# Performance work log

Hardware: AMD Instinct MI355X
Metric: run time of the kernel (lower is better)

The kernel has to match this reference:

```python
import jax, jax.numpy as jnp
import numpy as np

N_NODES = 20000
N_EDGES = 640000
D = 128


def setup_inputs() -> dict:
    key = jax.random.key(0)
    ks = jax.random.split(key, 8)
    scale = 1.0 / np.sqrt(D)
    x = jax.random.normal(ks[0], (N_NODES, D), dtype=jnp.float32)
    edge_index = jax.random.randint(ks[1], (2, N_EDGES), 0, N_NODES, dtype=jnp.int64)
    W1_rel = jax.random.normal(ks[2], (D, D), dtype=jnp.float32) * scale
    b1_rel = jnp.zeros((D,), dtype=jnp.float32)
    W1_root = jax.random.normal(ks[3], (D, D), dtype=jnp.float32) * scale
    W2_rel = jax.random.normal(ks[4], (D, D), dtype=jnp.float32) * scale
    b2_rel = jnp.zeros((D,), dtype=jnp.float32)
    W2_root = jax.random.normal(ks[5], (D, D), dtype=jnp.float32) * scale
    return {"x": x, "edge_index": edge_index,
            "W1_rel": W1_rel, "b1_rel": b1_rel, "W1_root": W1_root,
            "W2_rel": W2_rel, "b2_rel": b2_rel, "W2_root": W2_root}


def _graph_conv(x, src, dst, W_rel, b_rel, W_root):
    # sum-aggregate neighbor features: gather from src, scatter-add to dst
    agg = jax.ops.segment_sum(x[src], dst, num_segments=N_NODES)  # [N, D]
    # PyG GraphConv: lin_rel(agg) (with bias) + lin_root(x) (no bias)
    return agg @ W_rel + b_rel + x @ W_root


def reference(x, edge_index, W1_rel, b1_rel, W1_root, W2_rel, b2_rel, W2_root):
    src, dst = edge_index[0], edge_index[1]  # messages flow src (j) -> dst (i)
    h = jax.nn.relu(_graph_conv(x, src, dst, W1_rel, b1_rel, W1_root))
    out = _graph_conv(h, src, dst, W2_rel, b2_rel, W2_root)  # final ReLU stripped
    return out
```

## Files before the change

### kernel.cpp

```cpp
#include <hip/hip_runtime.h>

#define N_NODES 20000
#define N_EDGES 640000
#define D 128
#define CAP 128

typedef __attribute__((ext_vector_type(8))) short bf16x8;
typedef __attribute__((ext_vector_type(4))) float f32x4;

__device__ __forceinline__ short f2bf(float f) {
    union { float f; unsigned u; } un; un.f = f;
    unsigned r = un.u + 0x7fff + ((un.u >> 16) & 1);
    return (short)(r >> 16);
}
__device__ __forceinline__ float bflo(unsigned u) { return __uint_as_float(u << 16); }
__device__ __forceinline__ float bfhi(unsigned u) { return __uint_as_float(u & 0xffff0000u); }

__global__ __launch_bounds__(256) void prep_kernel(
    const float* __restrict__ x,
    const int* __restrict__ src, const int* __restrict__ dst,
    const float* __restrict__ W1_rel, const float* __restrict__ W1_root,
    const float* __restrict__ W2_rel, const float* __restrict__ W2_root,
    int* __restrict__ cnt, unsigned short* __restrict__ buckets,
    short* __restrict__ xb, short* __restrict__ wpk1, short* __restrict__ wpk2)
{
    const int b = blockIdx.x;
    const int tid = threadIdx.x;
    if (b < 625) {
        int e4 = b * 256 + tid;
        int4 s4 = ((const int4*)src)[e4];
        int4 d4 = ((const int4*)dst)[e4];
#pragma unroll
        for (int q = 0; q < 4; q++) {
            int d = (&d4.x)[q];
            int s = (&s4.x)[q];
            int p = atomicAdd(&cnt[d], 1);
            if (p < CAP) buckets[(d << 7) + p] = (unsigned short)s;
        }
    } else if (b < 3125) {
        int i = (b - 625) * 256 + tid;
        float4 v = ((const float4*)x)[i];
        ushort4 o;
        o.x = (unsigned short)f2bf(v.x);
        o.y = (unsigned short)f2bf(v.y);
        o.z = (unsigned short)f2bf(v.z);
        o.w = (unsigned short)f2bf(v.w);
        ((ushort4*)xb)[i] = o;
    } else {
        int pb  = b - 3125;
        int job = pb >> 4;
        int idx = (pb & 15) * 256 + tid;
        const float* Wrel  = job ? W2_rel  : W1_rel;
        const float* Wroot = job ? W2_root : W1_root;
        short* Wpk = job ? wpk2 : wpk1;
        int lane = idx & 63;
        int ct   = (idx >> 6) & 7;
        int t    = idx >> 9;
        const float* W = (t < 4) ? Wrel : Wroot;
        int k0  = (t & 3) * 32 + (lane >> 4) * 8;
        int col = ct * 16 + (lane & 15);
        bf16x8 pk;
#pragma unroll
        for (int j = 0; j < 8; j++)
            pk[j] = f2bf(W[(size_t)(k0 + j) * D + col]);
        ((bf16x8*)Wpk)[idx] = pk;
    }
}

__global__ __launch_bounds__(256) void aggregate_kernel(
    const short* __restrict__ xb,
    const int* __restrict__ cnt,
    const unsigned short* __restrict__ buckets,
    short* __restrict__ aggb)
{
    int node = blockIdx.x * 8 + (threadIdx.x >> 5);
    int lane = threadIdx.x & 31;
    int n = cnt[node];
    n = (n > CAP) ? CAP : n;
    uint2 idxpk = *(const uint2*)(buckets + (node << 7) + lane * 4);

    float4 acc = make_float4(0.f, 0.f, 0.f, 0.f);
    int i = 0;
    for (; i + 8 <= n; i += 8) {
        int baseLane = i >> 2;
        uint2 u[8];
#pragma unroll
        for (int q = 0; q < 8; q++) {
            unsigned word = __shfl((q & 2) ? idxpk.y : idxpk.x,
                                   baseLane + (q >> 2), 32);
            unsigned sidx = (q & 1) ? (word >> 16) : (word & 0xffffu);
            u[q] = *(const uint2*)(xb + (size_t)sidx * D + lane * 4);
        }
#pragma unroll
        for (int q = 0; q < 8; q++) {
            acc.x += bflo(u[q].x); acc.y += bfhi(u[q].x);
            acc.z += bflo(u[q].y); acc.w += bfhi(u[q].y);
        }
    }
    for (; i < n; i++) {
        unsigned word = __shfl((i & 2) ? idxpk.y : idxpk.x, i >> 2, 32);
        unsigned sidx = (i & 1) ? (word >> 16) : (word & 0xffffu);
        uint2 u0 = *(const uint2*)(xb + (size_t)sidx * D + lane * 4);
        acc.x += bflo(u0.x); acc.y += bfhi(u0.x);
        acc.z += bflo(u0.y); acc.w += bfhi(u0.y);
    }
    ushort4 o;
    o.x = (unsigned short)f2bf(acc.x);
    o.y = (unsigned short)f2bf(acc.y);
    o.z = (unsigned short)f2bf(acc.z);
    o.w = (unsigned short)f2bf(acc.w);
    *(ushort4*)(aggb + (size_t)node * D + lane * 4) = o;
}

template <bool RELU, bool OUT_BF16>
__global__ __launch_bounds__(128) void gemm_kernel(
    const short* __restrict__ aggb,
    const short* __restrict__ xb,
    const short* __restrict__ Wpk,
    const float* __restrict__ brel,
    void* __restrict__ outp)
{
    const int tid  = threadIdx.x;
    const int wave = tid >> 6;
    const int lane = tid & 63;
    const int quad = lane >> 4;
    const int l16  = lane & 15;
    const int row0 = blockIdx.x * 32 + wave * 16;

    f32x4 acc[8];
#pragma unroll
    for (int ct = 0; ct < 8; ct++) acc[ct] = (f32x4){0.f, 0.f, 0.f, 0.f};

    const short* arow_agg = aggb + (size_t)(row0 + l16) * D + quad * 8;
    const short* arow_x   = xb   + (size_t)(row0 + l16) * D + quad * 8;
    const bf16x8* wb = (const bf16x8*)Wpk + lane;

#pragma unroll
    for (int t = 0; t < 8; t++) {
        const short* arow = (t < 4) ? arow_agg : arow_x;
        bf16x8 a = *(const bf16x8*)(arow + (t & 3) * 32);
        const bf16x8* wt = wb + (size_t)t * 8 * 64;
#pragma unroll
        for (int ct = 0; ct < 8; ct++) {
            bf16x8 bfr = wt[ct * 64];
            acc[ct] = __builtin_amdgcn_mfma_f32_16x16x32_bf16(a, bfr, acc[ct], 0, 0, 0);
        }
    }

    const int orow = row0 + quad * 4;
#pragma unroll
    for (int ct = 0; ct < 8; ct++) {
        const int col = ct * 16 + l16;
        const float bias = brel[col];
#pragma unroll
        for (int r = 0; r < 4; r++) {
            float v = acc[ct][r] + bias;
            if (RELU) v = fmaxf(v, 0.f);
            if (OUT_BF16)
                ((short*)outp)[(size_t)(orow + r) * D + col] = f2bf(v);
            else
                ((float*)outp)[(size_t)(orow + r) * D + col] = v;
        }
    }
}

extern "C" void kernel_launch(void* const* d_in, const int* in_sizes, int n_in,
                              void* d_out, int out_size, void* d_ws, size_t ws_size,
                              hipStream_t stream) {
    const float* x       = (const float*)d_in[0];
    const int*   ei      = (const int*)  d_in[1];
    const float* W1_rel  = (const float*)d_in[2];
    const float* b1_rel  = (const float*)d_in[3];
    const float* W1_root = (const float*)d_in[4];
    const float* W2_rel  = (const float*)d_in[5];
    const float* b2_rel  = (const float*)d_in[6];
    const float* W2_root = (const float*)d_in[7];
    float* out = (float*)d_out;

    char* p = (char*)d_ws;
    short* xb   = (short*)p;  p += (size_t)N_NODES * D * 2;
    short* hb   = (short*)p;  p += (size_t)N_NODES * D * 2;
    short* aggb = (short*)p;  p += (size_t)N_NODES * D * 2;
    short* wpk1 = (short*)p;  p += 65536;
    short* wpk2 = (short*)p;  p += 65536;
    int*   cnt  = (int*)p;    p += (size_t)N_NODES * 4;
    unsigned short* buckets = (unsigned short*)p;

    const int* src = ei;
    const int* dst = ei + N_EDGES;

    const int aggblocks  = N_NODES / 8;
    const int gemmblocks = N_NODES / 32;

    hipMemsetAsync(cnt, 0, (size_t)N_NODES * sizeof(int), stream);
    prep_kernel<<<3157, 256, 0, stream>>>(
        x, src, dst, W1_rel, W1_root, W2_rel, W2_root,
        cnt, buckets, xb, wpk1, wpk2);

    aggregate_kernel<<<aggblocks, 256, 0, stream>>>(xb, cnt, buckets, aggb);
    gemm_kernel<true, true><<<gemmblocks, 128, 0, stream>>>(
        aggb, xb, wpk1, b1_rel, (void*)hb);

    aggregate_kernel<<<aggblocks, 256, 0, stream>>>(hb, cnt, buckets, aggb);
    gemm_kernel<false, false><<<gemmblocks, 128, 0, stream>>>(
        aggb, hb, wpk2, b2_rel, (void*)out);
}
```

Before: 162.7 us.

## Fuse neighbor aggregation and GEMM into one per-layer kernel via LDS

Merges the aggregate and GEMM kernels into a single layer kernel. Each 512-thread block aggregates 16 nodes into shared memory, then 8 waves each compute one 16-column tile with MFMA. This removes the aggb round trip through global memory and two kernel launches. In exchange it adds a block-wide barrier between the gather and MFMA phases, and gives each wave fewer MFMAs, so the weight fragments are reloaded per block of 16 rows.

```diff
diff --git a/kernel.cpp b/kernel.cpp
--- a/kernel.cpp
+++ b/kernel.cpp
@@ -67,100 +67,93 @@
     }
 }
 
-__global__ __launch_bounds__(256) void aggregate_kernel(
-    const short* __restrict__ xb,
+template <bool RELU, bool OUT_BF16>
+__global__ __launch_bounds__(512) void layer_kernel(
+    const short* __restrict__ xin,
     const int* __restrict__ cnt,
     const unsigned short* __restrict__ buckets,
-    short* __restrict__ aggb)
-{
-    int node = blockIdx.x * 8 + (threadIdx.x >> 5);
-    int lane = threadIdx.x & 31;
-    int n = cnt[node];
-    n = (n > CAP) ? CAP : n;
-    uint2 idxpk = *(const uint2*)(buckets + (node << 7) + lane * 4);
-
-    float4 acc = make_float4(0.f, 0.f, 0.f, 0.f);
-    int i = 0;
-    for (; i + 8 <= n; i += 8) {
-        int baseLane = i >> 2;
-        uint2 u[8];
-#pragma unroll
-        for (int q = 0; q < 8; q++) {
-            unsigned word = __shfl((q & 2) ? idxpk.y : idxpk.x,
-                                   baseLane + (q >> 2), 32);
-            unsigned sidx = (q & 1) ? (word >> 16) : (word & 0xffffu);
-            u[q] = *(const uint2*)(xb + (size_t)sidx * D + lane * 4);
-        }
-#pragma unroll
-        for (int q = 0; q < 8; q++) {
-            acc.x += bflo(u[q].x); acc.y += bfhi(u[q].x);
-            acc.z += bflo(u[q].y); acc.w += bfhi(u[q].y);
-        }
-    }
-    for (; i < n; i++) {
-        unsigned word = __shfl((i & 2) ? idxpk.y : idxpk.x, i >> 2, 32);
-        unsigned sidx = (i & 1) ? (word >> 16) : (word & 0xffffu);
-        uint2 u0 = *(const uint2*)(xb + (size_t)sidx * D + lane * 4);
-        acc.x += bflo(u0.x); acc.y += bfhi(u0.x);
-        acc.z += bflo(u0.y); acc.w += bfhi(u0.y);
-    }
-    ushort4 o;
-    o.x = (unsigned short)f2bf(acc.x);
-    o.y = (unsigned short)f2bf(acc.y);
-    o.z = (unsigned short)f2bf(acc.z);
-    o.w = (unsigned short)f2bf(acc.w);
-    *(ushort4*)(aggb + (size_t)node * D + lane * 4) = o;
-}
-
-template <bool RELU, bool OUT_BF16>
-__global__ __launch_bounds__(128) void gemm_kernel(
-    const short* __restrict__ aggb,
-    const short* __restrict__ xb,
     const short* __restrict__ Wpk,
     const float* __restrict__ brel,
     void* __restrict__ outp)
 {
+    __shared__ short sAgg[16][136];
+
     const int tid  = threadIdx.x;
+    const int row0 = blockIdx.x * 16;
+
+    {
+        const int hw   = tid >> 5;
+        const int lane = tid & 31;
+        const int node = row0 + hw;
+        int n = cnt[node];
+        n = (n > CAP) ? CAP : n;
+        uint2 idxpk = *(const uint2*)(buckets + (node << 7) + lane * 4);
+
+        float4 acc = make_float4(0.f, 0.f, 0.f, 0.f);
+        int i = 0;
+        for (; i + 8 <= n; i += 8) {
+            int baseLane = i >> 2;
+            uint2 u[8];
+#pragma unroll
+            for (int q = 0; q < 8; q++) {
+                unsigned word = __shfl((q & 2) ? idxpk.y : idxpk.x,
+                                       baseLane + (q >> 2), 32);
+                unsigned sidx = (q & 1) ? (word >> 16) : (word & 0xffffu);
+                u[q] = *(const uint2*)(xin + (size_t)sidx * D + lane * 4);
+            }
+#pragma unroll
+            for (int q = 0; q < 8; q++) {
+                acc.x += bflo(u[q].x); acc.y += bfhi(u[q].x);
+                acc.z += bflo(u[q].y); acc.w += bfhi(u[q].y);
+            }
+        }
+        for (; i < n; i++) {
+            unsigned word = __shfl((i & 2) ? idxpk.y : idxpk.x, i >> 2, 32);
+            unsigned sidx = (i & 1) ? (word >> 16) : (word & 0xffffu);
+            uint2 u0 = *(const uint2*)(xin + (size_t)sidx * D + lane * 4);
+            acc.x += bflo(u0.x); acc.y += bfhi(u0.x);
+            acc.z += bflo(u0.y); acc.w += bfhi(u0.y);
+        }
+        ushort4 o;
+        o.x = (unsigned short)f2bf(acc.x);
+        o.y = (unsigned short)f2bf(acc.y);
+        o.z = (unsigned short)f2bf(acc.z);
+        o.w = (unsigned short)f2bf(acc.w);
+        *(ushort4*)&sAgg[hw][lane * 4] = o;
+    }
+    __syncthreads();
+
     const int wave = tid >> 6;
     const int lane = tid & 63;
     const int quad = lane >> 4;
     const int l16  = lane & 15;
-    const int row0 = blockIdx.x * 32 + wave * 16;
 
-    f32x4 acc[8];
-#pragma unroll
-    for (int ct = 0; ct < 8; ct++) acc[ct] = (f32x4){0.f, 0.f, 0.f, 0.f};
-
-    const short* arow_agg = aggb + (size_t)(row0 + l16) * D + quad * 8;
-    const short* arow_x   = xb   + (size_t)(row0 + l16) * D + quad * 8;
+    f32x4 acc = (f32x4){0.f, 0.f, 0.f, 0.f};
+    const short* arow_x = xin + (size_t)(row0 + l16) * D + quad * 8;
     const bf16x8* wb = (const bf16x8*)Wpk + lane;
 
 #pragma unroll
     for (int t = 0; t < 8; t++) {
-        const short* arow = (t < 4) ? arow_agg : arow_x;
-        bf16x8 a = *(const bf16x8*)(arow + (t & 3) * 32);
-        const bf16x8* wt = wb + (size_t)t * 8 * 64;
-#pragma unroll
-        for (int ct = 0; ct < 8; ct++) {
-            bf16x8 bfr = wt[ct * 64];
-            acc[ct] = __builtin_amdgcn_mfma_f32_16x16x32_bf16(a, bfr, acc[ct], 0, 0, 0);
-        }
+        bf16x8 a;
+        if (t < 4)
+            a = *(const bf16x8*)&sAgg[l16][(t & 3) * 32 + quad * 8];
+        else
+            a = *(const bf16x8*)(arow_x + (t & 3) * 32);
+        bf16x8 bfr = wb[(t * 8 + wave) * 64];
+        acc = __builtin_amdgcn_mfma_f32_16x16x32_bf16(a, bfr, acc, 0, 0, 0);
     }
 
+    const int col  = wave * 16 + l16;
     const int orow = row0 + quad * 4;
+    const float bias = brel[col];
 #pragma unroll
-    for (int ct = 0; ct < 8; ct++) {
-        const int col = ct * 16 + l16;
-        const float bias = brel[col];
-#pragma unroll
-        for (int r = 0; r < 4; r++) {
-            float v = acc[ct][r] + bias;
-            if (RELU) v = fmaxf(v, 0.f);
-            if (OUT_BF16)
-                ((short*)outp)[(size_t)(orow + r) * D + col] = f2bf(v);
-            else
-                ((float*)outp)[(size_t)(orow + r) * D + col] = v;
-        }
+    for (int r = 0; r < 4; r++) {
+        float v = acc[r] + bias;
+        if (RELU) v = fmaxf(v, 0.f);
+        if (OUT_BF16)
+            ((short*)outp)[(size_t)(orow + r) * D + col] = f2bf(v);
+        else
+            ((float*)outp)[(size_t)(orow + r) * D + col] = v;
     }
 }
 
@@ -180,7 +173,6 @@
     char* p = (char*)d_ws;
     short* xb   = (short*)p;  p += (size_t)N_NODES * D * 2;
     short* hb   = (short*)p;  p += (size_t)N_NODES * D * 2;
-    short* aggb = (short*)p;  p += (size_t)N_NODES * D * 2;
     short* wpk1 = (short*)p;  p += 65536;
     short* wpk2 = (short*)p;  p += 65536;
     int*   cnt  = (int*)p;    p += (size_t)N_NODES * 4;
@@ -189,19 +181,16 @@
     const int* src = ei;
     const int* dst = ei + N_EDGES;
 
-    const int aggblocks  = N_NODES / 8;
-    const int gemmblocks = N_NODES / 32;
+    const int layerblocks = N_NODES / 16;
 
     hipMemsetAsync(cnt, 0, (size_t)N_NODES * sizeof(int), stream);
     prep_kernel<<<3157, 256, 0, stream>>>(
         x, src, dst, W1_rel, W1_root, W2_rel, W2_root,
         cnt, buckets, xb, wpk1, wpk2);
 
-    aggregate_kernel<<<aggblocks, 256, 0, stream>>>(xb, cnt, buckets, aggb);
-    gemm_kernel<true, true><<<gemmblocks, 128, 0, stream>>>(
-        aggb, xb, wpk1, b1_rel, (void*)hb);
+    layer_kernel<true, true><<<layerblocks, 512, 0, stream>>>(
+        xb, cnt, buckets, wpk1, b1_rel, (void*)hb);
 
-    aggregate_kernel<<<aggblocks, 256, 0, stream>>>(hb, cnt, buckets, aggb);
-    gemm_kernel<false, false><<<gemmblocks, 128, 0, stream>>>(
-        aggb, hb, wpk2, b2_rel, (void*)out);
+    layer_kernel<false, false><<<layerblocks, 512, 0, stream>>>(
+        hb, cnt, buckets, wpk2, b2_rel, (void*)out);
 }
```

Result: no change. 160.0 us (-1.6%).
